# Kernel optimization log

Measured on AMD Instinct MI355X. Metric: run time of the kernel, lower is better.

## Reference

```python
import jax, jax.numpy as jnp
import numpy as np

LN_EPS = 1e-5      # torch layer_norm default eps
L2_EPS = 1e-12     # torch F.normalize default eps
SM_EPS = 1e-12
TAU = 1.0          # self.tau set in __init__
ROW_FLOOR = 0.05
ROW_CEILING = 0.35
NEG = -1e9


def _layer_norm(z):
    m = z.mean(axis=-1, keepdims=True)
    v = z.var(axis=-1, keepdims=True)
    return (z - m) / jnp.sqrt(v + LN_EPS)


def _l2_normalize(z):
    n = jnp.sqrt(jnp.sum(z * z, axis=-1, keepdims=True))
    return z / jnp.maximum(n, L2_EPS)


def setup_inputs() -> dict:
    key = jax.random.key(0)
    k1, k2, k3, k4, k5 = jax.random.split(key, 5)
    B, N, T, C, H = 16, 128, 512, 64, 64
    gain = 1.414
    bound = gain * np.sqrt(6.0 / (C + H))  # xavier_uniform with gain
    x = jax.random.normal(k1, (B, N, T, C), dtype=jnp.float32)
    Wq = jax.random.uniform(k2, (H, C), minval=-bound, maxval=bound, dtype=jnp.float32)
    Wk = jax.random.uniform(k3, (H, C), minval=-bound, maxval=bound, dtype=jnp.float32)
    bq = jax.random.uniform(k4, (H,), minval=-0.1, maxval=0.1, dtype=jnp.float32)
    bk = jax.random.uniform(k5, (H,), minval=-0.1, maxval=0.1, dtype=jnp.float32)
    return {"x": x, "Wq": Wq, "bq": bq, "Wk": Wk, "bk": bk, "band": 2}


def reference(x, Wq, bq, Wk, bk, band):
    B, N, T, C = x.shape
    x_mean = x.mean(axis=1)  # (B, T, C) -- reduce over nodes
    Q = _l2_normalize(_layer_norm(x_mean @ Wq.T + bq))  # (B, T, H)
    K = _l2_normalize(_layer_norm(x_mean @ Wk.T + bk))  # (B, T, H)
    logits = jnp.clip(jnp.einsum('bth,bsh->bts', Q, K), -6.0, 6.0)  # (B, T, T)

    idx = jnp.arange(T)
    dist = jnp.abs(idx[None, :] - idx[:, None])
    mask = (dist <= band) & (dist > 0)  # self_loop=False removes diagonal

    masked = jnp.where(mask[None, :, :], logits, NEG)
    masked = masked - jnp.max(masked, axis=-1, keepdims=True)
    A = jax.nn.softmax(masked / TAU, axis=-1)
    A = jnp.maximum(A, SM_EPS)
    A = (1.0 - ROW_FLOOR) * A + ROW_FLOOR / T
    A = jnp.minimum(A, ROW_CEILING)
    A = A / jnp.maximum(jnp.sum(A, axis=-1, keepdims=True), SM_EPS)
    A = A / jnp.maximum(jnp.sum(A, axis=-1, keepdims=True), SM_EPS)
    return A, logits
```

## Files before the change

kernel.cpp:

```cpp
#include <hip/hip_runtime.h>
#include <math.h>

#define BB 16
#define NN 128
#define TT 512
#define CC 64
#define HH 64

__device__ __forceinline__ float wsum64(float v) {
#pragma unroll
  for (int m = 1; m < 64; m <<= 1) v += __shfl_xor(v, m, 64);
  return v;
}

__global__ __launch_bounds__(256) void fused_mean_proj(
    const float* __restrict__ x, const float* __restrict__ Wq,
    const float* __restrict__ bq, const float* __restrict__ Wk,
    const float* __restrict__ bk, float* __restrict__ Qt,
    float* __restrict__ Kmat) {
  __shared__ float Wq_s[64 * 65];
  __shared__ float Wk_s[64 * 65];
  __shared__ float xm_s[16 * 64];
  __shared__ float qt_s[64 * 17];

  const int tid = threadIdx.x;
  const int b = blockIdx.x >> 5;
  const int t0 = (blockIdx.x & 31) << 4;

#pragma unroll
  for (int it = 0; it < 16; ++it) {
    int i = it * 256 + tid;
    int h = i >> 6, c = i & 63;
    Wq_s[c * 65 + h] = Wq[i];
    Wk_s[c * 65 + h] = Wk[i];
  }

  {
    const int j = tid >> 4;
    const int c4 = tid & 15;
    const float4* xp = (const float4*)x;
    size_t base4 = ((size_t)b * NN * TT + (size_t)(t0 + j)) * 16 + c4;
    float4 s = {0.f, 0.f, 0.f, 0.f};
#pragma unroll 8
    for (int n = 0; n < NN; ++n) {
      float4 v = xp[base4 + (size_t)n * (TT * 16)];
      s.x += v.x; s.y += v.y; s.z += v.z; s.w += v.w;
    }
    const float inv = 1.0f / (float)NN;
    float4 xm4;
    xm4.x = s.x * inv; xm4.y = s.y * inv; xm4.z = s.z * inv; xm4.w = s.w * inv;
    *(float4*)&xm_s[j * 64 + c4 * 4] = xm4;
  }
  __syncthreads();

  const int rw = tid >> 6;
  const int h = tid & 63;
  float qa[4], ka[4];
  const float bqv = bq[h], bkv = bk[h];
#pragma unroll
  for (int r = 0; r < 4; ++r) { qa[r] = bqv; ka[r] = bkv; }
#pragma unroll
  for (int c = 0; c < 64; ++c) {
    float wq = Wq_s[c * 65 + h];
    float wk = Wk_s[c * 65 + h];
#pragma unroll
    for (int r = 0; r < 4; ++r) {
      float xv = xm_s[(rw * 4 + r) * 64 + c];
      qa[r] = fmaf(xv, wq, qa[r]);
      ka[r] = fmaf(xv, wk, ka[r]);
    }
  }

#pragma unroll
  for (int r = 0; r < 4; ++r) {
    const int t = t0 + rw * 4 + r;
    float mq = wsum64(qa[r]) * (1.f / 64.f);
    float dq = qa[r] - mq;
    float vq = wsum64(dq * dq) * (1.f / 64.f);
    float yq = dq / sqrtf(vq + 1e-5f);
    float nq = sqrtf(wsum64(yq * yq));
    yq = yq / fmaxf(nq, 1e-12f);
    qt_s[h * 17 + rw * 4 + r] = yq;
    float mk = wsum64(ka[r]) * (1.f / 64.f);
    float dk = ka[r] - mk;
    float vk = wsum64(dk * dk) * (1.f / 64.f);
    float yk = dk / sqrtf(vk + 1e-5f);
    float nk = sqrtf(wsum64(yk * yk));
    yk = yk / fmaxf(nk, 1e-12f);
    Kmat[((size_t)b * TT + t) * HH + h] = yk;
  }
  __syncthreads();

  {
    const int hh = tid >> 2, part = tid & 3;
    float4 o;
    o.x = qt_s[hh * 17 + part * 4 + 0];
    o.y = qt_s[hh * 17 + part * 4 + 1];
    o.z = qt_s[hh * 17 + part * 4 + 2];
    o.w = qt_s[hh * 17 + part * 4 + 3];
    *(float4*)&Qt[((size_t)b * HH + hh) * TT + t0 + part * 4] = o;
  }
}

__global__ __launch_bounds__(256) void logits_kernel(
    const float* __restrict__ Qt, const float* __restrict__ Kmat,
    float* __restrict__ logits) {
  const int lane = threadIdx.x & 63;
  const int w = threadIdx.x >> 6;
  const int b = blockIdx.x >> 6;
  const int rem = blockIdx.x & 63;
  const int rg = rem >> 1;
  const int half = rem & 1;
  const int r0 = rg * 16;
  const int cg = half * 4 + w;
  const int scol = cg * 64 + lane;

  const float4* kp = (const float4*)(Kmat + ((size_t)b * TT + scol) * HH);
  float4 kv[16];
#pragma unroll
  for (int i = 0; i < 16; ++i) kv[i] = kp[i];

  float acc[16];
#pragma unroll
  for (int r = 0; r < 16; ++r) acc[r] = 0.f;

  const float* qtb = Qt + (size_t)b * HH * TT + r0;
#pragma unroll
  for (int c4 = 0; c4 < 16; ++c4) {
    float4 k4 = kv[c4];
    const float* q0 = qtb + (size_t)(4 * c4 + 0) * TT;
    const float* q1 = qtb + (size_t)(4 * c4 + 1) * TT;
    const float* q2 = qtb + (size_t)(4 * c4 + 2) * TT;
    const float* q3 = qtb + (size_t)(4 * c4 + 3) * TT;
#pragma unroll
    for (int r = 0; r < 16; ++r) {
      acc[r] = fmaf(q0[r], k4.x, acc[r]);
      acc[r] = fmaf(q1[r], k4.y, acc[r]);
      acc[r] = fmaf(q2[r], k4.z, acc[r]);
      acc[r] = fmaf(q3[r], k4.w, acc[r]);
    }
  }

  float* lrow = logits + ((size_t)b * TT + r0) * TT + cg * 64 + lane;
#pragma unroll
  for (int r = 0; r < 16; ++r) {
    float v = fminf(fmaxf(acc[r], -6.f), 6.f);
    lrow[(size_t)r * TT] = v;
  }
}

__global__ __launch_bounds__(256) void adj_kernel(
    const float* __restrict__ logits, const int* __restrict__ bandp,
    float* __restrict__ A) {
  const int w = threadIdx.x >> 6, lane = threadIdx.x & 63;
  const int row = blockIdx.x * 4 + w;
  const int t = row & (TT - 1);
  const int band = *bandp;
  const float* lrow = logits + (size_t)row * TT;

  float mx = -3.0e38f;
  for (int jj = -band; jj <= band; ++jj) {
    if (jj == 0) continue;
    int ss = t + jj;
    if (ss < 0 || ss >= TT) continue;
    mx = fmaxf(mx, lrow[ss]);
  }
  float den = 0.f;
  int nb = 0;
  for (int jj = -band; jj <= band; ++jj) {
    if (jj == 0) continue;
    int ss = t + jj;
    if (ss < 0 || ss >= TT) continue;
    den += expf(lrow[ss] - mx);
    ++nb;
  }
  const float fl = 0.05f / (float)TT;
  const float offa = 0.95f * 1e-12f + fl;
  float bsum = 0.f;
  for (int jj = -band; jj <= band; ++jj) {
    if (jj == 0) continue;
    int ss = t + jj;
    if (ss < 0 || ss >= TT) continue;
    float p = expf(lrow[ss] - mx) / den;
    float a = fminf(0.95f * p + fl, 0.35f);
    bsum += a;
  }
  const float s1 = fmaxf(bsum + (float)(TT - nb) * offa, 1e-12f);
  const float off1 = offa / s1;
  float bsum1 = 0.f;
  for (int jj = -band; jj <= band; ++jj) {
    if (jj == 0) continue;
    int ss = t + jj;
    if (ss < 0 || ss >= TT) continue;
    float p = expf(lrow[ss] - mx) / den;
    float a = fminf(0.95f * p + fl, 0.35f);
    bsum1 += a / s1;
  }
  const float s2 = fmaxf(bsum1 + (float)(TT - nb) * off1, 1e-12f);
  const float off2 = off1 / s2;

  auto colval = [&](int ss) -> float {
    int d = ss - t;
    if (d != 0 && d >= -band && d <= band) {
      float p = expf(lrow[ss] - mx) / den;
      float a = fminf(0.95f * p + fl, 0.35f);
      return a / s1 / s2;
    }
    return off2;
  };

  float* arow = A + (size_t)row * TT + lane * 8;
  const int cb = lane * 8;
  float4 o0, o1;
  o0.x = colval(cb + 0); o0.y = colval(cb + 1);
  o0.z = colval(cb + 2); o0.w = colval(cb + 3);
  o1.x = colval(cb + 4); o1.y = colval(cb + 5);
  o1.z = colval(cb + 6); o1.w = colval(cb + 7);
  *(float4*)&arow[0] = o0;
  *(float4*)&arow[4] = o1;
}

extern "C" void kernel_launch(void* const* d_in, const int* in_sizes, int n_in,
                              void* d_out, int out_size, void* d_ws, size_t ws_size,
                              hipStream_t stream) {
  (void)in_sizes; (void)n_in; (void)out_size; (void)ws_size;
  const float* x  = (const float*)d_in[0];
  const float* Wq = (const float*)d_in[1];
  const float* bq = (const float*)d_in[2];
  const float* Wk = (const float*)d_in[3];
  const float* bk = (const float*)d_in[4];
  const int* band = (const int*)d_in[5];

  float* A = (float*)d_out;
  float* logits = A + (size_t)BB * TT * TT;
  float* Qt = (float*)d_ws;
  float* Kmat = Qt + (size_t)BB * HH * TT;

  fused_mean_proj<<<512, 256, 0, stream>>>(x, Wq, bq, Wk, bk, Qt, Kmat);
  logits_kernel<<<1024, 256, 0, stream>>>(Qt, Kmat, logits);
  adj_kernel<<<2048, 256, 0, stream>>>(logits, band, A);
}
```

Baseline: 99.86 us.

## Split node-mean reduction into separate high-parallelism kernel before projection

The mean over nodes moves out of the fused projection kernel into its own kernel with 2048 blocks. Each block covers 4 timesteps, and its four waves each sum 32 of the 128 nodes, then combine the partial sums through shared memory. The intent is more memory-level parallelism on the large 268MB read of x, which was limited to 512 blocks with 128 serial loads per thread. The cost is an extra launch plus a workspace round-trip for xmean.

```diff
diff --git a/kernel.cpp b/kernel.cpp
--- a/kernel.cpp
+++ b/kernel.cpp
@@ -13,8 +13,38 @@
   return v;
 }
 
-__global__ __launch_bounds__(256) void fused_mean_proj(
-    const float* __restrict__ x, const float* __restrict__ Wq,
+__global__ __launch_bounds__(256) void mean_kernel(
+    const float* __restrict__ x, float* __restrict__ xmean) {
+  const int tid = threadIdx.x;
+  const int b = blockIdx.x >> 7;
+  const int t0 = (blockIdx.x & 127) << 2;
+  const int w = tid >> 6;
+  const int lane = tid & 63;
+  const int j = lane >> 4;
+  const int c4 = lane & 15;
+
+  const float4* xp = (const float4*)x;
+  size_t base4 = ((size_t)b * NN * TT + (size_t)(t0 + j)) * 16 + c4 +
+                 (size_t)(w * 32) * (TT * 16);
+  float4 s = {0.f, 0.f, 0.f, 0.f};
+#pragma unroll 8
+  for (int n = 0; n < 32; ++n) {
+    float4 v = xp[base4 + (size_t)n * (TT * 16)];
+    s.x += v.x; s.y += v.y; s.z += v.z; s.w += v.w;
+  }
+
+  __shared__ float red[4][4][64];
+  *(float4*)&red[w][j][c4 * 4] = s;
+  __syncthreads();
+
+  const int jj = tid >> 6, cc = tid & 63;
+  float m = (red[0][jj][cc] + red[1][jj][cc] + red[2][jj][cc] +
+             red[3][jj][cc]) * (1.f / 128.f);
+  xmean[((size_t)b * TT + t0 + jj) * CC + cc] = m;
+}
+
+__global__ __launch_bounds__(256) void proj_kernel(
+    const float* __restrict__ xmean, const float* __restrict__ Wq,
     const float* __restrict__ bq, const float* __restrict__ Wk,
     const float* __restrict__ bk, float* __restrict__ Qt,
     float* __restrict__ Kmat) {
@@ -34,23 +64,7 @@
     Wq_s[c * 65 + h] = Wq[i];
     Wk_s[c * 65 + h] = Wk[i];
   }
-
-  {
-    const int j = tid >> 4;
-    const int c4 = tid & 15;
-    const float4* xp = (const float4*)x;
-    size_t base4 = ((size_t)b * NN * TT + (size_t)(t0 + j)) * 16 + c4;
-    float4 s = {0.f, 0.f, 0.f, 0.f};
-#pragma unroll 8
-    for (int n = 0; n < NN; ++n) {
-      float4 v = xp[base4 + (size_t)n * (TT * 16)];
-      s.x += v.x; s.y += v.y; s.z += v.z; s.w += v.w;
-    }
-    const float inv = 1.0f / (float)NN;
-    float4 xm4;
-    xm4.x = s.x * inv; xm4.y = s.y * inv; xm4.z = s.z * inv; xm4.w = s.w * inv;
-    *(float4*)&xm_s[j * 64 + c4 * 4] = xm4;
-  }
+  ((float4*)xm_s)[tid] = ((const float4*)(xmean + ((size_t)b * TT + t0) * CC))[tid];
   __syncthreads();
 
   const int rw = tid >> 6;
@@ -81,6 +95,7 @@
     float nq = sqrtf(wsum64(yq * yq));
     yq = yq / fmaxf(nq, 1e-12f);
     qt_s[h * 17 + rw * 4 + r] = yq;
+
     float mk = wsum64(ka[r]) * (1.f / 64.f);
     float dk = ka[r] - mk;
     float vk = wsum64(dk * dk) * (1.f / 64.f);
@@ -233,10 +248,12 @@
 
   float* A = (float*)d_out;
   float* logits = A + (size_t)BB * TT * TT;
-  float* Qt = (float*)d_ws;
+  float* xmean = (float*)d_ws;
+  float* Qt = xmean + (size_t)BB * TT * CC;
   float* Kmat = Qt + (size_t)BB * HH * TT;
 
-  fused_mean_proj<<<512, 256, 0, stream>>>(x, Wq, bq, Wk, bk, Qt, Kmat);
+  mean_kernel<<<2048, 256, 0, stream>>>(x, xmean);
+  proj_kernel<<<512, 256, 0, stream>>>(xmean, Wq, bq, Wk, bk, Qt, Kmat);
   logits_kernel<<<1024, 256, 0, stream>>>(Qt, Kmat, logits);
   adj_kernel<<<2048, 256, 0, stream>>>(logits, band, A);
 }
```

Measured after the change: 100.4 us. About the same (+0.5%).
